# Kernel tuning notes

Measured on AMD Instinct MI355X. Metric: run time of the kernel, lower is better.

The kernel has to match this reference:

```python
import jax, jax.numpy as jnp
import numpy as np

BATCH, SEQ_LEN, HIDDEN, NUM_SENTS = 16, 4096, 1024, 32


def setup_inputs() -> dict:
    key = jax.random.key(0)
    k1, k2 = jax.random.split(key)
    last_hidden_state = jax.random.normal(k1, (BATCH, SEQ_LEN, HIDDEN), dtype=jnp.float32)
    sentence_mask = jax.random.randint(k2, (BATCH, SEQ_LEN), 0, NUM_SENTS, dtype=jnp.int64)
    return {
        "last_hidden_state": last_hidden_state,
        "sentence_mask": sentence_mask,
        "num_sents": NUM_SENTS,
    }


def reference(last_hidden_state, sentence_mask, num_sents):
    # unique sentence ids; assume ids 0..num_sents-1 all occur (static shape)
    unique_sents = jnp.arange(num_sents, dtype=sentence_mask.dtype)
    # one-hot segment membership: (batch, num_sents, seq_len)
    masks = (sentence_mask[:, None, :] == unique_sents[None, :, None])
    counts = masks.sum(axis=2).astype(last_hidden_state.dtype)  # (batch, num_sents)
    # segment-sum via contraction over seq_len -> (batch, num_sents, hidden);
    # avoids the torch (B, S, L, H) broadcasted intermediate
    sums = jnp.einsum("bsl,blh->bsh", masks.astype(last_hidden_state.dtype), last_hidden_state)
    sentence_embeddings = sums / counts[:, :, None]
    return sentence_embeddings, unique_sents
```

## Files before the change

### kernel.cpp

```cpp
#include <hip/hip_runtime.h>


#define BATCH   16
#define SEQ     4096
#define HIDDEN  1024
#define NSENT   32
#define CHUNK   256
#define NCHUNK  (HIDDEN / CHUNK)
#define KSPLIT  8
#define SEG     (SEQ / KSPLIT)
#define EMB_ELEMS (BATCH * NSENT * HIDDEN)

__global__ __launch_bounds__(256) void count_kernel(const int* __restrict__ mask,
                                                    float* __restrict__ counts) {
    __shared__ int c[NSENT];
    const int b   = blockIdx.x;
    const int tid = threadIdx.x;
    if (tid < NSENT) c[tid] = 0;
    __syncthreads();
    for (int i = tid; i < SEQ; i += 256) {
        atomicAdd(&c[mask[b * SEQ + i] & (NSENT - 1)], 1);
    }
    __syncthreads();
    if (tid < NSENT) counts[b * NSENT + tid] = (float)c[tid];
}

__global__ __launch_bounds__(256) void accum_kernel(const float* __restrict__ x,
                                                    const int* __restrict__ mask,
                                                    float* __restrict__ sums) {
    __shared__ float acc[NSENT][CHUNK];
    __shared__ int   smask[SEG];

    const int tid   = threadIdx.x;
    const int blk   = blockIdx.x;
    const int b     = blk / (NCHUNK * KSPLIT);
    const int rem   = blk % (NCHUNK * KSPLIT);
    const int chunk = rem / KSPLIT;
    const int split = rem % KSPLIT;

    #pragma unroll
    for (int s = 0; s < NSENT; ++s) acc[s][tid] = 0.0f;

    const int l0 = split * SEG;
    for (int i = tid; i < SEG; i += 256)
        smask[i] = mask[b * SEQ + l0 + i] & (NSENT - 1);
    __syncthreads();

    const float* xp = x + (size_t)(b * SEQ + l0) * HIDDEN + chunk * CHUNK + tid;
    #pragma unroll 8
    for (int i = 0; i < SEG; ++i) {
        acc[smask[i]][tid] += xp[(size_t)i * HIDDEN];
    }
    __syncthreads();

    float* dst = sums + (size_t)b * NSENT * HIDDEN + chunk * CHUNK + tid;
    #pragma unroll
    for (int s = 0; s < NSENT; ++s) {
        atomicAdd(dst + s * HIDDEN, acc[s][tid]);
    }
}

__global__ __launch_bounds__(256) void finalize_kernel(float* __restrict__ out,
                                                       const float* __restrict__ counts) {
    const int idx = blockIdx.x * 256 + threadIdx.x;
    const float c = counts[idx >> 10];
    out[idx] = out[idx] / c;
    if (idx < NSENT) out[EMB_ELEMS + idx] = (float)idx;
}

extern "C" void kernel_launch(void* const* d_in, const int* in_sizes, int n_in,
                              void* d_out, int out_size, void* d_ws, size_t ws_size,
                              hipStream_t stream) {
    const float* x    = (const float*)d_in[0];
    const int*   mask = (const int*)d_in[1];
    float*       out  = (float*)d_out;
    float*       counts = (float*)d_ws;

    hipMemsetAsync(out, 0, (size_t)EMB_ELEMS * sizeof(float), stream);

    count_kernel<<<BATCH, 256, 0, stream>>>(mask, counts);
    accum_kernel<<<BATCH * NCHUNK * KSPLIT, 256, 0, stream>>>(x, mask, out);
    finalize_kernel<<<EMB_ELEMS / 256, 256, 0, stream>>>(out, counts);
}
```

Before: 374.2 us.

## Use float4 loads, per-split partial buffers, and fuse counting into accumulation

Restructures the segment-sum so each block covers a 512-wide hidden chunk over a 256-row split, loading x as float4 and accumulating into shared memory with LDS atomics, since two row-groups now share the accumulator. Each block writes its partial sums and counts to a workspace instead of issuing global atomics. A finalize kernel reduces the 16 partials and divides by the summed counts, which removes the memset and the separate count kernel. The trade-off is extra workspace traffic (16x the output size) plus shared-memory atomic contention, in exchange for wider global loads and no global atomics.

Result: slower. 605.7 us (+61.9%).

```diff
diff --git a/kernel.cpp b/kernel.cpp
--- a/kernel.cpp
+++ b/kernel.cpp
@@ -5,80 +5,100 @@
 #define SEQ     4096
 #define HIDDEN  1024
 #define NSENT   32
-#define CHUNK   256
-#define NCHUNK  (HIDDEN / CHUNK)
-#define KSPLIT  8
+#define NCHUNK  2
+#define CHUNK   (HIDDEN / NCHUNK)
+#define KSPLIT  16
 #define SEG     (SEQ / KSPLIT)
 #define EMB_ELEMS (BATCH * NSENT * HIDDEN)
+#define PARTIAL_ELEMS ((size_t)KSPLIT * EMB_ELEMS)
 
-__global__ __launch_bounds__(256) void count_kernel(const int* __restrict__ mask,
-                                                    float* __restrict__ counts) {
-    __shared__ int c[NSENT];
-    const int b   = blockIdx.x;
-    const int tid = threadIdx.x;
-    if (tid < NSENT) c[tid] = 0;
-    __syncthreads();
-    for (int i = tid; i < SEQ; i += 256) {
-        atomicAdd(&c[mask[b * SEQ + i] & (NSENT - 1)], 1);
-    }
-    __syncthreads();
-    if (tid < NSENT) counts[b * NSENT + tid] = (float)c[tid];
-}
+__global__ __launch_bounds__(256) void accum_kernel(const float4* __restrict__ x4,
+                                                    const int* __restrict__ mask,
+                                                    float* __restrict__ partial,
+                                                    float* __restrict__ pcounts) {
+    __shared__ float acc[NSENT * CHUNK];
+    __shared__ int   smask[SEG];
+    __shared__ int   scnt[NSENT];
 
-__global__ __launch_bounds__(256) void accum_kernel(const float* __restrict__ x,
-                                                    const int* __restrict__ mask,
-                                                    float* __restrict__ sums) {
-    __shared__ float acc[NSENT][CHUNK];
-    __shared__ int   smask[SEG];
+    const int tid    = threadIdx.x;
+    const int blk    = blockIdx.x;
+    const int b      = blk >> 5;
+    const int rem    = blk & 31;
+    const int hchunk = rem >> 4;
+    const int split  = rem & 15;
 
-    const int tid   = threadIdx.x;
-    const int blk   = blockIdx.x;
-    const int b     = blk / (NCHUNK * KSPLIT);
-    const int rem   = blk % (NCHUNK * KSPLIT);
-    const int chunk = rem / KSPLIT;
-    const int split = rem % KSPLIT;
+    const int pair = tid >> 7;
+    const int tpos = tid & 127;
 
     #pragma unroll
-    for (int s = 0; s < NSENT; ++s) acc[s][tid] = 0.0f;
-
-    const int l0 = split * SEG;
-    for (int i = tid; i < SEG; i += 256)
-        smask[i] = mask[b * SEQ + l0 + i] & (NSENT - 1);
+    for (int i = tid; i < NSENT * CHUNK; i += 256) acc[i] = 0.0f;
+    if (tid < NSENT) scnt[tid] = 0;
     __syncthreads();
 
-    const float* xp = x + (size_t)(b * SEQ + l0) * HIDDEN + chunk * CHUNK + tid;
-    #pragma unroll 8
-    for (int i = 0; i < SEG; ++i) {
-        acc[smask[i]][tid] += xp[(size_t)i * HIDDEN];
+    {
+        int m = mask[b * SEQ + split * SEG + tid] & (NSENT - 1);
+        smask[tid] = m;
+        atomicAdd(&scnt[m], 1);
     }
     __syncthreads();
 
-    float* dst = sums + (size_t)b * NSENT * HIDDEN + chunk * CHUNK + tid;
+    const float4* xp = x4 + (size_t)(b * SEQ + split * SEG) * (HIDDEN / 4)
+                          + hchunk * (CHUNK / 4) + tpos;
+    #pragma unroll 8
+    for (int r = pair; r < SEG; r += 2) {
+        float4 v = xp[(size_t)r * (HIDDEN / 4)];
+        const int s = smask[r];
+        float* a = &acc[s * CHUNK + tpos];
+        atomicAdd(a,       v.x);
+        atomicAdd(a + 128, v.y);
+        atomicAdd(a + 256, v.z);
+        atomicAdd(a + 384, v.w);
+    }
+    __syncthreads();
+
+    float* dst = partial + (size_t)(split * BATCH + b) * NSENT * HIDDEN + hchunk * CHUNK;
     #pragma unroll
-    for (int s = 0; s < NSENT; ++s) {
-        atomicAdd(dst + s * HIDDEN, acc[s][tid]);
+    for (int s0 = 0; s0 < NSENT; s0 += 2) {
+        const int s = s0 + pair;
+        float4 v;
+        v.x = acc[s * CHUNK + tpos];
+        v.y = acc[s * CHUNK + 128 + tpos];
+        v.z = acc[s * CHUNK + 256 + tpos];
+        v.w = acc[s * CHUNK + 384 + tpos];
+        ((float4*)(dst + (size_t)s * HIDDEN))[tpos] = v;
     }
+    if (hchunk == 0 && tid < NSENT)
+        pcounts[(split * BATCH + b) * NSENT + tid] = (float)scnt[tid];
 }
 
-__global__ __launch_bounds__(256) void finalize_kernel(float* __restrict__ out,
-                                                       const float* __restrict__ counts) {
-    const int idx = blockIdx.x * 256 + threadIdx.x;
-    const float c = counts[idx >> 10];
-    out[idx] = out[idx] / c;
-    if (idx < NSENT) out[EMB_ELEMS + idx] = (float)idx;
+__global__ __launch_bounds__(256) void finalize_kernel(const float4* __restrict__ partial4,
+                                                       const float* __restrict__ pcounts,
+                                                       float* __restrict__ out) {
+    const int i4 = blockIdx.x * 256 + threadIdx.x;
+    const int bs = i4 >> 8;
+    float  cnt = 0.0f;
+    float4 sum = {0.0f, 0.0f, 0.0f, 0.0f};
+    #pragma unroll
+    for (int sp = 0; sp < KSPLIT; ++sp) {
+        float4 v = partial4[(size_t)sp * (EMB_ELEMS / 4) + i4];
+        sum.x += v.x; sum.y += v.y; sum.z += v.z; sum.w += v.w;
+        cnt += pcounts[sp * (BATCH * NSENT) + bs];
+    }
+    float4 o = {sum.x / cnt, sum.y / cnt, sum.z / cnt, sum.w / cnt};
+    ((float4*)out)[i4] = o;
+    if (i4 < NSENT) out[EMB_ELEMS + i4] = (float)i4;
 }
 
 extern "C" void kernel_launch(void* const* d_in, const int* in_sizes, int n_in,
                               void* d_out, int out_size, void* d_ws, size_t ws_size,
                               hipStream_t stream) {
-    const float* x    = (const float*)d_in[0];
-    const int*   mask = (const int*)d_in[1];
-    float*       out  = (float*)d_out;
-    float*       counts = (float*)d_ws;
+    const float4* x4   = (const float4*)d_in[0];
+    const int*    mask = (const int*)d_in[1];
+    float*        out  = (float*)d_out;
 
-    hipMemsetAsync(out, 0, (size_t)EMB_ELEMS * sizeof(float), stream);
+    float* partial = (float*)d_ws;
+    float* pcounts = (float*)d_ws + PARTIAL_ELEMS;
 
-    count_kernel<<<BATCH, 256, 0, stream>>>(mask, counts);
-    accum_kernel<<<BATCH * NCHUNK * KSPLIT, 256, 0, stream>>>(x, mask, out);
-    finalize_kernel<<<EMB_ELEMS / 256, 256, 0, stream>>>(out, counts);
+    accum_kernel<<<BATCH * NCHUNK * KSPLIT, 256, 0, stream>>>(x4, mask, partial, pcounts);
+    finalize_kernel<<<EMB_ELEMS / 4 / 256, 256, 0, stream>>>((const float4*)partial, pcounts, out);
 }
```
